# Optimization experiments

Measured on AMD Instinct MI355X. Metric: run time of the kernel, lower is better.

Reference implementation:

```python
import jax, jax.numpy as jnp
import numpy as np

D, H, F, L, V = 768, 4, 1024, 3, 10000
B, TLAB, S = 16, 513, 197
SCALE = 0.02


def setup_inputs() -> dict:
    key = jax.random.key(0)
    ks = jax.random.split(key, 16)
    inp = {
        'labels': jax.random.randint(ks[0], (B, TLAB), 0, V),
        'vision_feats': jax.random.normal(ks[1], (B, S, D), jnp.float32),
        'vis_proj_w': jax.random.normal(ks[2], (D, D), jnp.float32) * SCALE,
        'vis_proj_b': jnp.zeros((D,), jnp.float32),
        'tok_emb': jax.random.normal(ks[3], (V, D), jnp.float32) * SCALE,
        'pos_emb': jax.random.normal(ks[4], (1, 512, D), jnp.float32) * SCALE,
        'sa_w': jax.random.normal(ks[5], (L, 3 * D, D), jnp.float32) * SCALE,
        'sa_b': jnp.zeros((L, 3 * D), jnp.float32),
        'sa_out_w': jax.random.normal(ks[6], (L, D, D), jnp.float32) * SCALE,
        'sa_out_b': jnp.zeros((L, D), jnp.float32),
        'ca_w': jax.random.normal(ks[7], (L, 3 * D, D), jnp.float32) * SCALE,
        'ca_b': jnp.zeros((L, 3 * D), jnp.float32),
        'ca_out_w': jax.random.normal(ks[8], (L, D, D), jnp.float32) * SCALE,
        'ca_out_b': jnp.zeros((L, D), jnp.float32),
        'ln1_g': jnp.ones((L, D), jnp.float32), 'ln1_b': jnp.zeros((L, D), jnp.float32),
        'ln2_g': jnp.ones((L, D), jnp.float32), 'ln2_b': jnp.zeros((L, D), jnp.float32),
        'ln3_g': jnp.ones((L, D), jnp.float32), 'ln3_b': jnp.zeros((L, D), jnp.float32),
        'ff1_w': jax.random.normal(ks[9], (L, F, D), jnp.float32) * SCALE,
        'ff1_b': jnp.zeros((L, F), jnp.float32),
        'ff2_w': jax.random.normal(ks[10], (L, D, F), jnp.float32) * SCALE,
        'ff2_b': jnp.zeros((L, D), jnp.float32),
        'out_w': jax.random.normal(ks[11], (V, D), jnp.float32) * SCALE,
        'out_b': jnp.zeros((V,), jnp.float32),
    }
    return inp


def layer_norm(x, g, b, eps=1e-5):
    m = jnp.mean(x, axis=-1, keepdims=True)
    v = jnp.var(x, axis=-1, keepdims=True)
    return (x - m) / jnp.sqrt(v + eps) * g + b


def mha(qx, kx, vx, w, b, ow, ob, mask):
    # torch nn.MultiheadAttention with packed in_proj [3D, D]
    d = qx.shape[-1]
    hd = d // H
    q = qx @ w[:d].T + b[:d]
    k = kx @ w[d:2 * d].T + b[d:2 * d]
    v = vx @ w[2 * d:].T + b[2 * d:]
    def split(t):
        return t.reshape(t.shape[0], t.shape[1], H, hd).transpose(0, 2, 1, 3)
    q, k, v = split(q), split(k), split(v)  # [B,H,T,hd]
    s = jnp.einsum('bhqd,bhkd->bhqk', q, k) / jnp.sqrt(jnp.asarray(hd, qx.dtype))
    if mask is not None:
        s = s + mask
    a = jax.nn.softmax(s, axis=-1)
    o = jnp.einsum('bhqk,bhkd->bhqd', a, v)
    o = o.transpose(0, 2, 1, 3).reshape(qx.shape[0], qx.shape[1], d)
    return o @ ow.T + ob


def decode(labels, vision_feats, vis_proj_w, vis_proj_b, tok_emb, pos_emb,
           sa_w, sa_b, sa_out_w, sa_out_b, ca_w, ca_b, ca_out_w, ca_out_b,
           ln1_g, ln1_b, ln2_g, ln2_b, ln3_g, ln3_b,
           ff1_w, ff1_b, ff2_w, ff2_b, out_w, out_b):
    mem = vision_feats @ vis_proj_w.T + vis_proj_b          # [B,S,D]
    tgt_tok = labels[:, :-1]                                # [B,T] T=512
    T = tgt_tok.shape[1]
    x = tok_emb[tgt_tok] + pos_emb[:, :T, :]                # [B,T,D]
    # causal additive mask (teacher-forced loop == single full causal pass)
    mask = jnp.where(jnp.tril(jnp.ones((T, T), bool)), 0.0, -jnp.inf).astype(x.dtype)
    for l in range(L):
        x = layer_norm(x + mha(x, x, x, sa_w[l], sa_b[l], sa_out_w[l], sa_out_b[l], mask), ln1_g[l], ln1_b[l])
        x = layer_norm(x + mha(x, mem, mem, ca_w[l], ca_b[l], ca_out_w[l], ca_out_b[l], None), ln2_g[l], ln2_b[l])
        ff = jax.nn.relu(x @ ff1_w[l].T + ff1_b[l]) @ ff2_w[l].T + ff2_b[l]
        x = layer_norm(x + ff, ln3_g[l], ln3_b[l])
    return x @ out_w.T + out_b                              # [B,T,V]


def reference(labels, vision_feats, vis_proj_w, vis_proj_b, tok_emb, pos_emb,
              sa_w, sa_b, sa_out_w, sa_out_b, ca_w, ca_b, ca_out_w, ca_out_b,
              ln1_g, ln1_b, ln2_g, ln2_b, ln3_g, ln3_b,
              ff1_w, ff1_b, ff2_w, ff2_b, out_w, out_b):
    logits = decode(labels, vision_feats, vis_proj_w, vis_proj_b, tok_emb, pos_emb,
                    sa_w, sa_b, sa_out_w, sa_out_b, ca_w, ca_b, ca_out_w, ca_out_b,
                    ln1_g, ln1_b, ln2_g, ln2_b, ln3_g, ln3_b,
                    ff1_w, ff1_b, ff2_w, ff2_b, out_w, out_b)
    return (logits, labels[:, 1:])
```

## Files before the change

kernel.cpp:

```cpp
#include <hip/hip_runtime.h>
#include <hip/hip_fp8.h>

typedef unsigned short u16;
typedef __bf16 bf16x8 __attribute__((ext_vector_type(8)));
typedef float f32x4 __attribute__((ext_vector_type(4)));
typedef unsigned short u16x8 __attribute__((ext_vector_type(8)));
typedef unsigned short u16x4 __attribute__((ext_vector_type(4)));
typedef long i64;

typedef __attribute__((address_space(3))) u16 lds_u16_t;
typedef __attribute__((address_space(1))) const u16 glb_u16_t;
typedef __attribute__((address_space(3))) unsigned char lds_u8_t;
typedef __attribute__((address_space(1))) const unsigned char glb_u8_t;

__device__ __forceinline__ u16 f2bf(float f) {
    union { float f; unsigned u; } v; v.f = f;
    unsigned r = v.u + 0x7FFFu + ((v.u >> 16) & 1u);
    return (u16)(r >> 16);
}
__device__ __forceinline__ float bf2f(u16 h) {
    union { unsigned u; float f; } v; v.u = ((unsigned)h) << 16; return v.f;
}
__device__ __forceinline__ unsigned char f2e4m3(float f) {
    __hip_fp8_e4m3 h(f);
    return (unsigned char)h.__x;
}

struct Cast5 { const float* s[5]; u16* d[5]; long n4[5]; };
__global__ __launch_bounds__(256) void cast5_kernel(Cast5 a) {
    int seg = blockIdx.z;
    const float* s = a.s[seg];
    u16* d = a.d[seg];
    long n4 = a.n4[seg];
    long i = (long)blockIdx.x * 256 + threadIdx.x;
    long stride = (long)gridDim.x * 256;
    for (; i < n4; i += stride) {
        float4 f = reinterpret_cast<const float4*>(s)[i];
        ushort4 o;
        o.x = f2bf(f.x); o.y = f2bf(f.y); o.z = f2bf(f.z); o.w = f2bf(f.w);
        reinterpret_cast<ushort4*>(d)[i] = o;
    }
}
struct CastQ { const float* s[4]; unsigned char* d[4]; long n4[4]; };
__global__ __launch_bounds__(256) void castq_kernel(CastQ a) {
    int seg = blockIdx.z;
    const float* s = a.s[seg];
    unsigned char* d = a.d[seg];
    long n4 = a.n4[seg];
    long i = (long)blockIdx.x * 256 + threadIdx.x;
    long stride = (long)gridDim.x * 256;
    for (; i < n4; i += stride) {
        float4 f = reinterpret_cast<const float4*>(s)[i];
        uchar4 o;
        o.x = f2e4m3(f.x * 256.f); o.y = f2e4m3(f.y * 256.f);
        o.z = f2e4m3(f.z * 256.f); o.w = f2e4m3(f.w * 256.f);
        reinterpret_cast<uchar4*>(d)[i] = o;
    }
}

__global__ __launch_bounds__(256) void embed_kernel(
    const int* __restrict__ labels, const float* __restrict__ tok_emb,
    const float* __restrict__ pos_emb, u16* __restrict__ xb,
    unsigned char* __restrict__ xq, float* __restrict__ lab_out)
{
    int wid = threadIdx.x >> 6, lane = threadIdx.x & 63;
    int r = blockIdx.x * 4 + wid;
    int b = r >> 9, t = r & 511;
    int tok = labels[b * 513 + t];
    if (lane == 0) lab_out[r] = (float)labels[b * 513 + t + 1];
    const float* te = tok_emb + (long)tok * 768;
    const float* pe = pos_emb + (long)t * 768;
    u16* xo = xb + (long)r * 768;
    unsigned char* qo = xq + (long)r * 768;
    int base = lane * 12;
#pragma unroll
    for (int c = 0; c < 3; c++) {
        float4 a = *reinterpret_cast<const float4*>(te + base + c * 4);
        float4 p = *reinterpret_cast<const float4*>(pe + base + c * 4);
        float v0 = a.x + p.x, v1 = a.y + p.y, v2 = a.z + p.z, v3 = a.w + p.w;
        ushort4 o; o.x = f2bf(v0); o.y = f2bf(v1); o.z = f2bf(v2); o.w = f2bf(v3);
        *reinterpret_cast<ushort4*>(xo + base + c * 4) = o;
        uchar4 q; q.x = f2e4m3(v0); q.y = f2e4m3(v1); q.z = f2e4m3(v2); q.w = f2e4m3(v3);
        *reinterpret_cast<uchar4*>(qo + base + c * 4) = q;
    }
}

template<int OB, int RELU, int BM, int MW>
__global__ __launch_bounds__(256, MW) void gemmT(
    const u16* __restrict__ A, int lda, long sAb, long sAh,
    const u16* __restrict__ W, int ldw, long sWb, long sWh,
    const float* __restrict__ bias,
    void* __restrict__ C, int ldc, long sCb, long sCh,
    int M, int N, int K, int NH)
{
    constexpr int MREP = 4;
    constexpr int NREP = (BM == 128) ? 4 : 2;
    __shared__ __align__(16) u16 As0[BM * 32];
    __shared__ __align__(16) u16 As1[BM * 32];
    __shared__ __align__(16) u16 Bs0[128 * 32];
    __shared__ __align__(16) u16 Bs1[128 * 32];

    int z = blockIdx.z, zb = z / NH, zh = z % NH;
    const u16* Ap = A + (long)zb * sAb + (long)zh * sAh;
    const u16* Wp = W + (long)zb * sWb + (long)zh * sWh;
    long coff = (long)zb * sCb + (long)zh * sCh;

    int gx = (int)gridDim.x, gy = (int)gridDim.y;
    int nwg = gx * gy;
    int orig = (int)(blockIdx.y * gridDim.x + blockIdx.x);
    int q = nwg >> 3, r = nwg & 7;
    int xcd = orig & 7, loc = orig >> 3;
    int wg = (xcd < r ? xcd * (q + 1) : r * (q + 1) + (xcd - r) * q) + loc;
    int full = 8 * gy;
    int nsc = (gx + 7) >> 3;
    int sc = wg / full; if (sc > nsc - 1) sc = nsc - 1;
    int rem = wg - sc * full;
    int wdt = gx - sc * 8; if (wdt > 8) wdt = 8;
    int by = rem / wdt, bx = sc * 8 + rem % wdt;

    int m0 = by * BM, n0 = bx * 128;
    int tid = threadIdx.x, wid = tid >> 6, lane = tid & 63;
    int wr = (BM == 128) ? (wid >> 1) * 64 : 0;
    int wc = (BM == 128) ? (wid & 1) * 64 : wid * 32;
    int fr = lane & 15, fk = (lane >> 4) * 8;

    int li0 = wid * 64 + lane;
    int li1 = li0 + 256;
    int r0 = li0 >> 2, c0 = (li0 & 3) * 8;
    int r1 = li1 >> 2, c1 = (li1 & 3) * 8;
    long aoff0 = (long)min(m0 + r0, M - 1) * lda + c0;
    long aoff1 = (BM == 128) ? ((long)min(m0 + r1, M - 1) * lda + c1) : 0;
    long woff0 = (long)min(n0 + r0, N - 1) * ldw + c0;
    long woff1 = (long)min(n0 + r1, N - 1) * ldw + c1;
    char* a0base = (char*)As0 + wid * 1024;
    char* a1base = (char*)As1 + wid * 1024;
    char* b0base = (char*)Bs0 + wid * 1024;
    char* b1base = (char*)Bs1 + wid * 1024;

    f32x4 acc[MREP][NREP] = {};

    auto stage = [&](char* ab, char* bb, int kt) {
        int k0 = kt * 32;
        __builtin_amdgcn_global_load_lds((glb_u16_t*)(Ap + aoff0 + k0), (lds_u16_t*)ab, 16, 0, 0);
        if (BM == 128)
            __builtin_amdgcn_global_load_lds((glb_u16_t*)(Ap + aoff1 + k0), (lds_u16_t*)(ab + 4096), 16, 0, 0);
        __builtin_amdgcn_global_load_lds((glb_u16_t*)(Wp + woff0 + k0), (lds_u16_t*)bb, 16, 0, 0);
        __builtin_amdgcn_global_load_lds((glb_u16_t*)(Wp + woff1 + k0), (lds_u16_t*)(bb + 4096), 16, 0, 0);
    };
    auto compute = [&](const u16* as, const u16* bs) {
        bf16x8 af[MREP], bw[NREP];
#pragma unroll
        for (int m = 0; m < MREP; m++)
            af[m] = *reinterpret_cast<const bf16x8*>(&as[(wr + m * 16 + fr) * 32 + fk]);
#pragma unroll
        for (int n = 0; n < NREP; n++)
            bw[n] = *reinterpret_cast<const bf16x8*>(&bs[(wc + n * 16 + fr) * 32 + fk]);
#pragma unroll
        for (int m = 0; m < MREP; m++)
#pragma unroll
            for (int n = 0; n < NREP; n++)
                acc[m][n] = __builtin_amdgcn_mfma_f32_16x16x32_bf16(af[m], bw[n], acc[m][n], 0, 0, 0);
    };

    int nt = K >> 5;
    stage(a0base, b0base, 0);
    __syncthreads();
    for (int t = 0; t < nt; t += 2) {
        stage(a1base, b1base, t + 1);
        compute(As0, Bs0);
        __syncthreads();
        if (t + 2 < nt) stage(a0base, b0base, t + 2);
        compute(As1, Bs1);
        __syncthreads();
    }

    int crow = (lane >> 4) * 4;
#pragma unroll
    for (int m = 0; m < MREP; m++) {
#pragma unroll
        for (int n = 0; n < NREP; n++) {
            int col = n0 + wc + n * 16 + fr;
            if (col >= N) continue;
            float bv = bias ? bias[col] : 0.f;
            int rbase = m0 + wr + m * 16 + crow;
#pragma unroll
            for (int rr = 0; rr < 4; rr++) {
                int row = rbase + rr;
                if (row >= M) continue;
                float v = acc[m][n][rr] + bv;
                if (RELU) v = fmaxf(v, 0.f);
                long idx = coff + (long)row * ldc + col;
                if (OB) ((u16*)C)[idx] = f2bf(v);
                else    ((float*)C)[idx] = v;
            }
        }
    }
}

template<int OUT, int RELU>
__global__ __launch_bounds__(256, 4) void gemm8(
    const unsigned char* __restrict__ A, int lda,
    const unsigned char* __restrict__ W, int ldw,
    const float* __restrict__ bias, float outscale,
    void* __restrict__ C, int ldc,
    int M, int N, int K)
{
    __shared__ __align__(16) unsigned char As0[128 * 64];
    __shared__ __align__(16) unsigned char As1[128 * 64];
    __shared__ __align__(16) unsigned char Bs0[128 * 64];
    __shared__ __align__(16) unsigned char Bs1[128 * 64];

    int gx = (int)gridDim.x, gy = (int)gridDim.y;
    int nwg = gx * gy;
    int orig = (int)(blockIdx.y * gridDim.x + blockIdx.x);
    int q = nwg >> 3, r = nwg & 7;
    int xcd = orig & 7, loc = orig >> 3;
    int wg = (xcd < r ? xcd * (q + 1) : r * (q + 1) + (xcd - r) * q) + loc;
    int full = 8 * gy;
    int nsc = (gx + 7) >> 3;
    int sc = wg / full; if (sc > nsc - 1) sc = nsc - 1;
    int rem = wg - sc * full;
    int wdt = gx - sc * 8; if (wdt > 8) wdt = 8;
    int by = rem / wdt, bx = sc * 8 + rem % wdt;

    int m0 = by * 128, n0 = bx * 128;
    int tid = threadIdx.x, wid = tid >> 6, lane = tid & 63;
    int wr = (wid >> 1) * 64, wc = (wid & 1) * 64;
    int fr = lane & 15, g8 = (lane >> 4) * 8;

    int li0 = wid * 64 + lane;
    int rs = li0 >> 1;
    int cs = li0 & 1;
    int kc = ((cs ^ (rs >> 2)) & 1) << 4;
    long aoff = (long)min(m0 + rs, M - 1) * lda + kc;
    long woff = (long)min(n0 + rs, N - 1) * ldw + kc;
    char* a0base = (char*)As0 + wid * 1024;
    char* a1base = (char*)As1 + wid * 1024;
    char* b0base = (char*)Bs0 + wid * 1024;
    char* b1base = (char*)Bs1 + wid * 1024;

    f32x4 acc[4][4] = {};

    auto stage = [&](char* ab, char* bb, int kt) {
        int k0 = kt * 64;
        __builtin_amdgcn_global_load_lds((glb_u8_t*)(A + aoff + k0), (lds_u8_t*)ab, 16, 0, 0);
        __builtin_amdgcn_global_load_lds((glb_u8_t*)(A + aoff + k0 + 32), (lds_u8_t*)(ab + 4096), 16, 0, 0);
        __builtin_amdgcn_global_load_lds((glb_u8_t*)(W + woff + k0), (lds_u8_t*)bb, 16, 0, 0);
        __builtin_amdgcn_global_load_lds((glb_u8_t*)(W + woff + k0 + 32), (lds_u8_t*)(bb + 4096), 16, 0, 0);
    };
    int cg = g8 >> 4, go = g8 & 15;
    auto compute = [&](const unsigned char* as, const unsigned char* bs) {
        i64 af[4][2], bw[4][2];
#pragma unroll
        for (int m = 0; m < 4; m++) {
            int rr2 = wr + m * 16 + fr;
            int off = rr2 * 32 + (((cg ^ (rr2 >> 2)) & 1) << 4) + go;
            af[m][0] = *reinterpret_cast<const i64*>(as + off);
            af[m][1] = *reinterpret_cast<const i64*>(as + 4096 + off);
        }
#pragma unroll
        for (int n = 0; n < 4; n++) {
            int rr2 = wc + n * 16 + fr;
            int off = rr2 * 32 + (((cg ^ (rr2 >> 2)) & 1) << 4) + go;
            bw[n][0] = *reinterpret_cast<const i64*>(bs + off);
            bw[n][1] = *reinterpret_cast<const i64*>(bs + 4096 + off);
        }
#pragma unroll
        for (int ks = 0; ks < 2; ks++)
#pragma unroll
            for (int m = 0; m < 4; m++)
#pragma unroll
                for (int n = 0; n < 4; n++)
                    acc[m][n] = __builtin_amdgcn_mfma_f32_16x16x32_fp8_fp8(
                        af[m][ks], bw[n][ks], acc[m][n], 0, 0, 0);
    };

    int nt = K >> 6;
    stage(a0base, b0base, 0);
    __syncthreads();
    for (int t = 0; t < nt; t += 2) {
        stage(a1base, b1base, t + 1);
        compute(As0, Bs0);
        __syncthreads();
        if (t + 2 < nt) stage(a0base, b0base, t + 2);
        compute(As1, Bs1);
        __syncthreads();
    }

    int crow = (lane >> 4) * 4;
#pragma unroll
    for (int m = 0; m < 4; m++) {
#pragma unroll
        for (int n = 0; n < 4; n++) {
            int col = n0 + wc + n * 16 + fr;
            if (col >= N) continue;
            float bv = bias ? bias[col] : 0.f;
            int rbase = m0 + wr + m * 16 + crow;
#pragma unroll
            for (int rr = 0; rr < 4; rr++) {
                int row = rbase + rr;
                if (row >= M) continue;
                float v = acc[m][n][rr] * outscale + bv;
                if (RELU) v = fmaxf(v, 0.f);
                long idx = (long)row * ldc + col;
                if (OUT == 0)      ((float*)C)[idx] = v;
                else if (OUT == 1) ((u16*)C)[idx] = f2bf(v);
                else               ((unsigned char*)C)[idx] = f2e4m3(v);
            }
        }
    }
}

__global__ __launch_bounds__(256) void transpose_pad(
    const u16* __restrict__ V, long sVb, long sVh, int ldv, int NH,
    u16* __restrict__ VT, long sVT, int rowsIn, int Kp)
{
    __shared__ u16 tile[32][33];
    int z = blockIdx.z, zb = z / NH, zh = z % NH;
    const u16* Vp = V + (long)zb * sVb + (long)zh * sVh;
    int k0 = blockIdx.x * 32, d0 = blockIdx.y * 32;
#pragma unroll
    for (int i = 0; i < 4; i++) {
        int k = k0 + threadIdx.y + i * 8;
        int d = d0 + threadIdx.x;
        tile[threadIdx.y + i * 8][threadIdx.x] = (k < rowsIn) ? Vp[(long)k * ldv + d] : (u16)0;
    }
    __syncthreads();
    u16* Op = VT + (long)z * sVT;
#pragma unroll
    for (int i = 0; i < 4; i++) {
        int d = d0 + threadIdx.y + i * 8;
        int k = k0 + threadIdx.x;
        Op[(long)d * Kp + k] = tile[threadIdx.x][threadIdx.y + i * 8];
    }
}

template<int CPL, int CAUSAL>
__global__ __launch_bounds__(256) void softmax2(
    const u16* __restrict__ S, u16* __restrict__ P,
    int ld_in, int valid_in, int ld_out, float scale)
{
    int wid = threadIdx.x >> 6, lane = threadIdx.x & 63;
    long r = (long)blockIdx.x * 4 + wid;
    int q = (int)(r & 511);
    int valid = CAUSAL ? (q + 1) : valid_in;
    const u16* srow = S + r * (long)ld_in;
    u16* prow = P + r * (long)ld_out;
    int base = lane * CPL;
    float v[CPL];
    if constexpr (CPL == 8) {
        u16x8 x = *reinterpret_cast<const u16x8*>(srow + base);
#pragma unroll
        for (int j = 0; j < 8; j++) v[j] = bf2f(x[j]);
    } else {
        u16x4 x = *reinterpret_cast<const u16x4*>(srow + base);
#pragma unroll
        for (int j = 0; j < 4; j++) v[j] = bf2f(x[j]);
    }
    float mx = -3e38f;
#pragma unroll
    for (int j = 0; j < CPL; j++) {
        v[j] *= scale;
        if (base + j < valid) mx = fmaxf(mx, v[j]);
    }
#pragma unroll
    for (int o = 32; o; o >>= 1) mx = fmaxf(mx, __shfl_xor(mx, o, 64));
    float e[CPL], s = 0.f;
#pragma unroll
    for (int j = 0; j < CPL; j++) {
        e[j] = (base + j < valid) ? __expf(v[j] - mx) : 0.f;
        s += e[j];
    }
#pragma unroll
    for (int o = 32; o; o >>= 1) s += __shfl_xor(s, o, 64);
    float inv = 1.f / s;
    if constexpr (CPL == 8) {
        u16x8 o8;
#pragma unroll
        for (int j = 0; j < 8; j++) o8[j] = f2bf(e[j] * inv);
        *reinterpret_cast<u16x8*>(prow + base) = o8;
    } else {
        u16x4 o4;
#pragma unroll
        for (int j = 0; j < 4; j++) o4[j] = f2bf(e[j] * inv);
        *reinterpret_cast<u16x4*>(prow + base) = o4;
    }
}

__global__ __launch_bounds__(256) void ln_kernel(
    const u16* __restrict__ xin, const u16* __restrict__ subb,
    const float* __restrict__ g, const float* __restrict__ bta,
    u16* __restrict__ xout, unsigned char* __restrict__ q8)
{
    int wid = threadIdx.x >> 6, lane = threadIdx.x & 63;
    long r = (long)blockIdx.x * 4 + wid;
    const u16* a = xin + r * 768;
    const u16* s = subb + r * 768;
    int base = lane * 12;
    float v[12];
    float sum = 0.f;
#pragma unroll
    for (int c = 0; c < 3; c++) {
        ushort4 av = *reinterpret_cast<const ushort4*>(a + base + c * 4);
        ushort4 sv = *reinterpret_cast<const ushort4*>(s + base + c * 4);
        v[c*4+0] = bf2f(av.x) + bf2f(sv.x);
        v[c*4+1] = bf2f(av.y) + bf2f(sv.y);
        v[c*4+2] = bf2f(av.z) + bf2f(sv.z);
        v[c*4+3] = bf2f(av.w) + bf2f(sv.w);
        sum += v[c*4+0] + v[c*4+1] + v[c*4+2] + v[c*4+3];
    }
#pragma unroll
    for (int o = 32; o; o >>= 1) sum += __shfl_xor(sum, o, 64);
    float mean = sum * (1.f / 768.f);
    float vs = 0.f;
#pragma unroll
    for (int j = 0; j < 12; j++) { float t = v[j] - mean; vs += t * t; }
#pragma unroll
    for (int o = 32; o; o >>= 1) vs += __shfl_xor(vs, o, 64);
    float rstd = rsqrtf(vs * (1.f / 768.f) + 1e-5f);
    u16* xo = xout + r * 768;
    unsigned char* qo = q8 ? q8 + r * 768 : nullptr;
#pragma unroll
    for (int c = 0; c < 3; c++) {
        float4 gv = *reinterpret_cast<const float4*>(g + base + c * 4);
        float4 bv = *reinterpret_cast<const float4*>(bta + base + c * 4);
        float y0 = (v[c*4+0] - mean) * rstd * gv.x + bv.x;
        float y1 = (v[c*4+1] - mean) * rstd * gv.y + bv.y;
        float y2 = (v[c*4+2] - mean) * rstd * gv.z + bv.z;
        float y3 = (v[c*4+3] - mean) * rstd * gv.w + bv.w;
        ushort4 o; o.x = f2bf(y0); o.y = f2bf(y1); o.z = f2bf(y2); o.w = f2bf(y3);
        *reinterpret_cast<ushort4*>(xo + base + c * 4) = o;
        if (qo) {
            uchar4 qb; qb.x = f2e4m3(y0); qb.y = f2e4m3(y1); qb.z = f2e4m3(y2); qb.w = f2e4m3(y3);
            *reinterpret_cast<uchar4*>(qo + base + c * 4) = qb;
        }
    }
}

static void g128_bf(hipStream_t st, const u16* A, int lda, const u16* W, int ldw,
                    const float* bias, void* C, int ldc, int M, int N, int K) {
    dim3 g((N + 127) / 128, (M + 127) / 128, 1), b(256, 1, 1);
    gemmT<1,0,128,4><<<g,b,0,st>>>(A,lda,0,0,W,ldw,0,0,bias,C,ldc,0,0,M,N,K,1);
}
static void g64_bf(hipStream_t st, bool relu, const u16* A, int lda, const u16* W, int ldw,
                   const float* bias, void* C, int ldc, int M, int N, int K) {
    dim3 g((N + 127) / 128, (M + 63) / 64, 1), b(256, 1, 1);
    if (relu) gemmT<1,1,64,4><<<g,b,0,st>>>(A,lda,0,0,W,ldw,0,0,bias,C,ldc,0,0,M,N,K,1);
    else      gemmT<1,0,64,4><<<g,b,0,st>>>(A,lda,0,0,W,ldw,0,0,bias,C,ldc,0,0,M,N,K,1);
}
static void gbat(hipStream_t st,
    const u16* A, int lda, long sAb, long sAh,
    const u16* W, int ldw, long sWb, long sWh,
    void* C, int ldc, long sCb, long sCh,
    int M, int N, int K, int Z, int NH) {
    dim3 g((N + 127) / 128, (M + 127) / 128, Z), b(256, 1, 1);
    gemmT<1,0,128,4><<<g,b,0,st>>>(A,lda,sAb,sAh,W,ldw,sWb,sWh,nullptr,C,ldc,sCb,sCh,M,N,K,NH);
}
template<int OUT, int RELU>
static void g8(hipStream_t st, const unsigned char* A, int lda, const unsigned char* W, int ldw,
               const float* bias, void* C, int ldc, int M, int N, int K) {
    dim3 g((N + 127) / 128, (M + 127) / 128, 1), b(256, 1, 1);
    gemm8<OUT,RELU><<<g,b,0,st>>>(A,lda,W,ldw,bias,1.f/256.f,C,ldc,M,N,K);
}

extern "C" void kernel_launch(void* const* d_in, const int* in_sizes, int n_in,
                              void* d_out, int out_size, void* d_ws, size_t ws_size,
                              hipStream_t stream)
{
    const int*   labels = (const int*)  d_in[0];
    const float* vision = (const float*)d_in[1];
    const float* vpw    = (const float*)d_in[2];
    const float* vpb    = (const float*)d_in[3];
    const float* temb   = (const float*)d_in[4];
    const float* pemb   = (const float*)d_in[5];
    const float* saw    = (const float*)d_in[6];
    const float* sab    = (const float*)d_in[7];
    const float* saow   = (const float*)d_in[8];
    const float* saob   = (const float*)d_in[9];
    const float* caw    = (const float*)d_in[10];
    const float* cab    = (const float*)d_in[11];
    const float* caow   = (const float*)d_in[12];
    const float* caob   = (const float*)d_in[13];
    const float* ln1g   = (const float*)d_in[14];
    const float* ln1b   = (const float*)d_in[15];
    const float* ln2g   = (const float*)d_in[16];
    const float* ln2b   = (const float*)d_in[17];
    const float* ln3g   = (const float*)d_in[18];
    const float* ln3b   = (const float*)d_in[19];
    const float* f1w    = (const float*)d_in[20];
    const float* f1b    = (const float*)d_in[21];
    const float* f2w    = (const float*)d_in[22];
    const float* f2b    = (const float*)d_in[23];
    const float* ow     = (const float*)d_in[24];
    const float* ob     = (const float*)d_in[25];
    (void)in_sizes; (void)n_in; (void)out_size;

    char* p = (char*)d_ws;
    auto alloc = [&](long elems, int esz) -> char* {
        char* r = p; p += ((long)elems * esz + 255) & ~255L; return r;
    };
    u16* wb_vp  = (u16*)alloc(768L*768, 2);
    u16* wb_sao = (u16*)alloc(3L*768*768, 2);
    u16* wb_ca  = (u16*)alloc(3L*2304*768, 2);
    u16* wb_cao = (u16*)alloc(3L*768*768, 2);
    unsigned char* w8_sa = (unsigned char*)alloc(3L*2304*768, 1);
    unsigned char* w8_f1 = (unsigned char*)alloc(3L*1024*768, 1);
    unsigned char* w8_f2 = (unsigned char*)alloc(3L*768*1024, 1);
    unsigned char* w8_ow = (unsigned char*)alloc(10000L*768, 1);
    unsigned char* xq    = (unsigned char*)alloc(8192L*768, 1);
    unsigned char* h8    = (unsigned char*)alloc(8192L*1024, 1);
    u16* vis_b  = (u16*)alloc(3152L*768, 2);
    u16* mem_b  = (u16*)alloc(3152L*768, 2);
    u16* xb     = (u16*)alloc(8192L*768, 2);
    u16* qkv    = (u16*)alloc(8192L*2304, 2);
    u16* q_bf   = qkv;
    u16* kv_bf  = qkv + 8192L*768;
    u16* scb    = (u16*)alloc(64L*512*512, 2);
    u16* pr     = (u16*)alloc(64L*512*512, 2);
    u16* vt     = (u16*)alloc(64L*192*512, 2);
    u16* attn   = (u16*)alloc(8192L*768, 2);
    u16* subb   = (u16*)alloc(8192L*768, 2);
    if ((size_t)(p - (char*)d_ws) > ws_size) return;

    Cast5 c5;
    c5.s[0] = vpw;    c5.d[0] = wb_vp;  c5.n4[0] = 768L*768/4;
    c5.s[1] = saow;   c5.d[1] = wb_sao; c5.n4[1] = 3L*768*768/4;
    c5.s[2] = caw;    c5.d[2] = wb_ca;  c5.n4[2] = 3L*2304*768/4;
    c5.s[3] = caow;   c5.d[3] = wb_cao; c5.n4[3] = 3L*768*768/4;
    c5.s[4] = vision; c5.d[4] = vis_b;  c5.n4[4] = 3152L*768/4;
    cast5_kernel<<<dim3(512, 1, 5), dim3(256), 0, stream>>>(c5);
    CastQ cq;
    cq.s[0] = saw; cq.d[0] = w8_sa; cq.n4[0] = 3L*2304*768/4;
    cq.s[1] = f1w; cq.d[1] = w8_f1; cq.n4[1] = 3L*1024*768/4;
    cq.s[2] = f2w; cq.d[2] = w8_f2; cq.n4[2] = 3L*768*1024/4;
    cq.s[3] = ow;  cq.d[3] = w8_ow; cq.n4[3] = 10000L*768/4;
    castq_kernel<<<dim3(512, 1, 4), dim3(256), 0, stream>>>(cq);

    embed_kernel<<<dim3(2048), dim3(256), 0, stream>>>(labels, temb, pemb, xb, xq,
                                                       (float*)d_out + 81920000L);

    g64_bf(stream, false, vis_b, 768, wb_vp, 768, vpb, mem_b, 768, 3152, 768, 768);

    const float scale = 0.07216878364870323f;

    for (int l = 0; l < 3; l++) {
        g8<1,0>(stream, xq, 768, w8_sa + (long)l*2304*768, 768, sab + l*2304,
                qkv, 2304, 8192, 2304, 768);
        transpose_pad<<<dim3(16,6,64), dim3(32,8), 0, stream>>>(
            qkv + 1536, 512L*2304, 192L, 2304, 4, vt, 192L*512, 512, 512);
        gbat(stream, qkv, 2304, 512L*2304, 192, qkv + 768, 2304, 512L*2304, 192,
             scb, 512, 4L*512*512, 512L*512, 512, 512, 192, 64, 4);
        softmax2<8,1><<<dim3(8192), dim3(256), 0, stream>>>(scb, pr, 512, 512, 512, scale);
        gbat(stream, pr, 512, 4L*512*512, 512L*512, vt, 512, 4L*192*512, 192L*512,
             attn, 768, 512L*768, 192, 512, 192, 512, 64, 4);
        g64_bf(stream, false, attn, 768, wb_sao + (long)l*768*768, 768,
               saob + l*768, subb, 768, 8192, 768, 768);
        ln_kernel<<<dim3(2048), dim3(256), 0, stream>>>(xb, subb, ln1g + l*768, ln1b + l*768,
                                                        xb, nullptr);

        const u16* Wca = wb_ca + (long)l*2304*768;
        g64_bf(stream, false, xb, 768, Wca, 768, cab + l*2304, q_bf, 768, 8192, 768, 768);
        g64_bf(stream, false, mem_b, 768, Wca + 768L*768, 768, cab + l*2304 + 768,
               kv_bf, 1536, 3152, 1536, 768);
        transpose_pad<<<dim3(8,6,64), dim3(32,8), 0, stream>>>(
            kv_bf + 768, 197L*1536, 192L, 1536, 4, vt, 192L*256, 197, 256);
        gbat(stream, q_bf, 768, 512L*768, 192, kv_bf, 1536, 197L*1536, 192,
             scb, 224, 4L*512*224, 512L*224, 512, 197, 192, 64, 4);
        softmax2<4,0><<<dim3(8192), dim3(256), 0, stream>>>(scb, pr, 224, 197, 256, scale);
        gbat(stream, pr, 256, 4L*512*256, 512L*256, vt, 256, 4L*192*256, 192L*256,
             attn, 768, 512L*768, 192, 512, 192, 256, 64, 4);
        g64_bf(stream, false, attn, 768, wb_cao + (long)l*768*768, 768,
               caob + l*768, subb, 768, 8192, 768, 768);
        ln_kernel<<<dim3(2048), dim3(256), 0, stream>>>(xb, subb, ln2g + l*768, ln2b + l*768,
                                                        xb, xq);

        g8<2,1>(stream, xq, 768, w8_f1 + (long)l*1024*768, 768, f1b + l*1024,
                h8, 1024, 8192, 1024, 768);
        g8<1,0>(stream, h8, 1024, w8_f2 + (long)l*768*1024, 1024, f2b + l*768,
                subb, 768, 8192, 768, 1024);
        ln_kernel<<<dim3(2048), dim3(256), 0, stream>>>(xb, subb, ln3g + l*768, ln3b + l*768,
                                                        xb, xq);
    }

    g8<0,0>(stream, xq, 768, w8_ow, 768, ob, (float*)d_out, 10000, 8192, 10000, 768);
}
```

Baseline: 1.276 ms.

## Move remaining bf16 projection GEMMs to FP8 and fuse V-transpose into QKV epilogue

Converts the vision projection, self-attention output, cross-attention Q/KV and output projections from bf16 to FP8 GEMMs. All weights and the vision features are quantized in a single cast kernel. The attention PV GEMM now writes FP8 output directly so the following out-projection can consume it. The QKV GEMM epilogue also writes the transposed V, removing a separate transpose kernel, and a BM=64 variant is added to the FP8 GEMM for the narrower matrices. This cuts memory traffic and kernel launches at the cost of more quantization error in several layers.

```diff
diff --git a/kernel.cpp b/kernel.cpp
--- a/kernel.cpp
+++ b/kernel.cpp
@@ -26,34 +26,20 @@
     return (unsigned char)h.__x;
 }
 
-struct Cast5 { const float* s[5]; u16* d[5]; long n4[5]; };
-__global__ __launch_bounds__(256) void cast5_kernel(Cast5 a) {
-    int seg = blockIdx.z;
-    const float* s = a.s[seg];
-    u16* d = a.d[seg];
-    long n4 = a.n4[seg];
-    long i = (long)blockIdx.x * 256 + threadIdx.x;
-    long stride = (long)gridDim.x * 256;
-    for (; i < n4; i += stride) {
-        float4 f = reinterpret_cast<const float4*>(s)[i];
-        ushort4 o;
-        o.x = f2bf(f.x); o.y = f2bf(f.y); o.z = f2bf(f.z); o.w = f2bf(f.w);
-        reinterpret_cast<ushort4*>(d)[i] = o;
-    }
-}
-struct CastQ { const float* s[4]; unsigned char* d[4]; long n4[4]; };
+struct CastQ { const float* s[9]; unsigned char* d[9]; long n4[9]; float mul[9]; };
 __global__ __launch_bounds__(256) void castq_kernel(CastQ a) {
     int seg = blockIdx.z;
     const float* s = a.s[seg];
     unsigned char* d = a.d[seg];
     long n4 = a.n4[seg];
+    float mul = a.mul[seg];
     long i = (long)blockIdx.x * 256 + threadIdx.x;
     long stride = (long)gridDim.x * 256;
     for (; i < n4; i += stride) {
         float4 f = reinterpret_cast<const float4*>(s)[i];
         uchar4 o;
-        o.x = f2e4m3(f.x * 256.f); o.y = f2e4m3(f.y * 256.f);
-        o.z = f2e4m3(f.z * 256.f); o.w = f2e4m3(f.w * 256.f);
+        o.x = f2e4m3(f.x * mul); o.y = f2e4m3(f.y * mul);
+        o.z = f2e4m3(f.z * mul); o.w = f2e4m3(f.w * mul);
         reinterpret_cast<uchar4*>(d)[i] = o;
     }
 }
@@ -85,18 +71,15 @@
     }
 }
 
-template<int OB, int RELU, int BM, int MW>
-__global__ __launch_bounds__(256, MW) void gemmT(
+template<int OUT>
+__global__ __launch_bounds__(256, 4) void gemmT(
     const u16* __restrict__ A, int lda, long sAb, long sAh,
     const u16* __restrict__ W, int ldw, long sWb, long sWh,
-    const float* __restrict__ bias,
     void* __restrict__ C, int ldc, long sCb, long sCh,
     int M, int N, int K, int NH)
 {
-    constexpr int MREP = 4;
-    constexpr int NREP = (BM == 128) ? 4 : 2;
-    __shared__ __align__(16) u16 As0[BM * 32];
-    __shared__ __align__(16) u16 As1[BM * 32];
+    __shared__ __align__(16) u16 As0[128 * 32];
+    __shared__ __align__(16) u16 As1[128 * 32];
     __shared__ __align__(16) u16 Bs0[128 * 32];
     __shared__ __align__(16) u16 Bs1[128 * 32];
 
@@ -118,10 +101,9 @@
     int wdt = gx - sc * 8; if (wdt > 8) wdt = 8;
     int by = rem / wdt, bx = sc * 8 + rem % wdt;
 
-    int m0 = by * BM, n0 = bx * 128;
+    int m0 = by * 128, n0 = bx * 128;
     int tid = threadIdx.x, wid = tid >> 6, lane = tid & 63;
-    int wr = (BM == 128) ? (wid >> 1) * 64 : 0;
-    int wc = (BM == 128) ? (wid & 1) * 64 : wid * 32;
+    int wr = (wid >> 1) * 64, wc = (wid & 1) * 64;
     int fr = lane & 15, fk = (lane >> 4) * 8;
 
     int li0 = wid * 64 + lane;
@@ -129,7 +111,7 @@
     int r0 = li0 >> 2, c0 = (li0 & 3) * 8;
     int r1 = li1 >> 2, c1 = (li1 & 3) * 8;
     long aoff0 = (long)min(m0 + r0, M - 1) * lda + c0;
-    long aoff1 = (BM == 128) ? ((long)min(m0 + r1, M - 1) * lda + c1) : 0;
+    long aoff1 = (long)min(m0 + r1, M - 1) * lda + c1;
     long woff0 = (long)min(n0 + r0, N - 1) * ldw + c0;
     long woff1 = (long)min(n0 + r1, N - 1) * ldw + c1;
     char* a0base = (char*)As0 + wid * 1024;
@@ -137,28 +119,27 @@
     char* b0base = (char*)Bs0 + wid * 1024;
     char* b1base = (char*)Bs1 + wid * 1024;
 
-    f32x4 acc[MREP][NREP] = {};
+    f32x4 acc[4][4] = {};
 
     auto stage = [&](char* ab, char* bb, int kt) {
         int k0 = kt * 32;
         __builtin_amdgcn_global_load_lds((glb_u16_t*)(Ap + aoff0 + k0), (lds_u16_t*)ab, 16, 0, 0);
-        if (BM == 128)
-            __builtin_amdgcn_global_load_lds((glb_u16_t*)(Ap + aoff1 + k0), (lds_u16_t*)(ab + 4096), 16, 0, 0);
+        __builtin_amdgcn_global_load_lds((glb_u16_t*)(Ap + aoff1 + k0), (lds_u16_t*)(ab + 4096), 16, 0, 0);
         __builtin_amdgcn_global_load_lds((glb_u16_t*)(Wp + woff0 + k0), (lds_u16_t*)bb, 16, 0, 0);
         __builtin_amdgcn_global_load_lds((glb_u16_t*)(Wp + woff1 + k0), (lds_u16_t*)(bb + 4096), 16, 0, 0);
     };
     auto compute = [&](const u16* as, const u16* bs) {
-        bf16x8 af[MREP], bw[NREP];
-#pragma unroll
-        for (int m = 0; m < MREP; m++)
+        bf16x8 af[4], bw[4];
+#pragma unroll
+        for (int m = 0; m < 4; m++)
             af[m] = *reinterpret_cast<const bf16x8*>(&as[(wr + m * 16 + fr) * 32 + fk]);
 #pragma unroll
-        for (int n = 0; n < NREP; n++)
+        for (int n = 0; n < 4; n++)
             bw[n] = *reinterpret_cast<const bf16x8*>(&bs[(wc + n * 16 + fr) * 32 + fk]);
 #pragma unroll
-        for (int m = 0; m < MREP; m++)
-#pragma unroll
-            for (int n = 0; n < NREP; n++)
+        for (int m = 0; m < 4; m++)
+#pragma unroll
+            for (int n = 0; n < 4; n++)
                 acc[m][n] = __builtin_amdgcn_mfma_f32_16x16x32_bf16(af[m], bw[n], acc[m][n], 0, 0, 0);
     };
 
@@ -176,37 +157,37 @@
 
     int crow = (lane >> 4) * 4;
 #pragma unroll
-    for (int m = 0; m < MREP; m++) {
-#pragma unroll
-        for (int n = 0; n < NREP; n++) {
+    for (int m = 0; m < 4; m++) {
+#pragma unroll
+        for (int n = 0; n < 4; n++) {
             int col = n0 + wc + n * 16 + fr;
             if (col >= N) continue;
-            float bv = bias ? bias[col] : 0.f;
             int rbase = m0 + wr + m * 16 + crow;
 #pragma unroll
             for (int rr = 0; rr < 4; rr++) {
                 int row = rbase + rr;
                 if (row >= M) continue;
-                float v = acc[m][n][rr] + bv;
-                if (RELU) v = fmaxf(v, 0.f);
+                float v = acc[m][n][rr];
                 long idx = coff + (long)row * ldc + col;
-                if (OB) ((u16*)C)[idx] = f2bf(v);
-                else    ((float*)C)[idx] = v;
+                if (OUT == 1) ((u16*)C)[idx] = f2bf(v);
+                else          ((unsigned char*)C)[idx] = f2e4m3(v);
             }
         }
     }
 }
 
-template<int OUT, int RELU>
+template<int OUT, int RELU, int BM, int FUSEVT>
 __global__ __launch_bounds__(256, 4) void gemm8(
     const unsigned char* __restrict__ A, int lda,
     const unsigned char* __restrict__ W, int ldw,
     const float* __restrict__ bias, float outscale,
-    void* __restrict__ C, int ldc,
+    void* __restrict__ C, int ldc, u16* __restrict__ vt,
     int M, int N, int K)
 {
-    __shared__ __align__(16) unsigned char As0[128 * 64];
-    __shared__ __align__(16) unsigned char As1[128 * 64];
+    constexpr int NREP = (BM == 128) ? 4 : 2;
+    constexpr int AHALF = (BM == 128) ? 4096 : 2048;
+    __shared__ __align__(16) unsigned char As0[BM * 64];
+    __shared__ __align__(16) unsigned char As1[BM * 64];
     __shared__ __align__(16) unsigned char Bs0[128 * 64];
     __shared__ __align__(16) unsigned char Bs1[128 * 64];
 
@@ -223,43 +204,55 @@
     int wdt = gx - sc * 8; if (wdt > 8) wdt = 8;
     int by = rem / wdt, bx = sc * 8 + rem % wdt;
 
-    int m0 = by * 128, n0 = bx * 128;
+    int m0 = by * BM, n0 = bx * 128;
     int tid = threadIdx.x, wid = tid >> 6, lane = tid & 63;
-    int wr = (wid >> 1) * 64, wc = (wid & 1) * 64;
-    int fr = lane & 15, g8 = (lane >> 4) * 8;
+    int wr = (BM == 128) ? (wid >> 1) * 64 : 0;
+    int wc = (BM == 128) ? (wid & 1) * 64 : wid * 32;
+    int fr = lane & 15, gk = (lane >> 4) * 8;
 
     int li0 = wid * 64 + lane;
-    int rs = li0 >> 1;
-    int cs = li0 & 1;
-    int kc = ((cs ^ (rs >> 2)) & 1) << 4;
-    long aoff = (long)min(m0 + rs, M - 1) * lda + kc;
-    long woff = (long)min(n0 + rs, N - 1) * ldw + kc;
+    int rsW = li0 >> 1, csW = li0 & 1;
+    int kcW = ((csW ^ (rsW >> 2)) & 1) << 4;
+    long woff = (long)min(n0 + rsW, N - 1) * ldw + kcW;
+    long aoff;
+    if constexpr (BM == 128) {
+        aoff = (long)min(m0 + rsW, M - 1) * lda + kcW;
+    } else {
+        int halfA = li0 >> 7;
+        int rsA = (li0 >> 1) & 63, csA = li0 & 1;
+        int kcA = ((csA ^ (rsA >> 2)) & 1) << 4;
+        aoff = (long)min(m0 + rsA, M - 1) * lda + halfA * 32 + kcA;
+    }
     char* a0base = (char*)As0 + wid * 1024;
     char* a1base = (char*)As1 + wid * 1024;
     char* b0base = (char*)Bs0 + wid * 1024;
     char* b1base = (char*)Bs1 + wid * 1024;
 
-    f32x4 acc[4][4] = {};
+    f32x4 acc[4][NREP] = {};
 
     auto stage = [&](char* ab, char* bb, int kt) {
         int k0 = kt * 64;
-        __builtin_amdgcn_global_load_lds((glb_u8_t*)(A + aoff + k0), (lds_u8_t*)ab, 16, 0, 0);
-        __builtin_amdgcn_global_load_lds((glb_u8_t*)(A + aoff + k0 + 32), (lds_u8_t*)(ab + 4096), 16, 0, 0);
+        if constexpr (BM == 128) {
+            __builtin_amdgcn_global_load_lds((glb_u8_t*)(A + aoff + k0), (lds_u8_t*)ab, 16, 0, 0);
+            __builtin_amdgcn_global_load_lds((glb_u8_t*)(A + aoff + k0 + 32), (lds_u8_t*)(ab + 4096), 16, 0, 0);
+        } else {
+            __builtin_amdgcn_global_load_lds((glb_u8_t*)(A + aoff + k0), (lds_u8_t*)ab, 16, 0, 0);
+        }
         __builtin_amdgcn_global_load_lds((glb_u8_t*)(W + woff + k0), (lds_u8_t*)bb, 16, 0, 0);
         __builtin_amdgcn_global_load_lds((glb_u8_t*)(W + woff + k0 + 32), (lds_u8_t*)(bb + 4096), 16, 0, 0);
     };
-    int cg = g8 >> 4, go = g8 & 15;
+    int cg = gk >> 4, go = gk & 15;
     auto compute = [&](const unsigned char* as, const unsigned char* bs) {
-        i64 af[4][2], bw[4][2];
+        i64 af[4][2], bw[NREP][2];
 #pragma unroll
         for (int m = 0; m < 4; m++) {
             int rr2 = wr + m * 16 + fr;
             int off = rr2 * 32 + (((cg ^ (rr2 >> 2)) & 1) << 4) + go;
             af[m][0] = *reinterpret_cast<const i64*>(as + off);
-            af[m][1] = *reinterpret_cast<const i64*>(as + 4096 + off);
+            af[m][1] = *reinterpret_cast<const i64*>(as + AHALF + off);
         }
 #pragma unroll
-        for (int n = 0; n < 4; n++) {
+        for (int n = 0; n < NREP; n++) {
             int rr2 = wc + n * 16 + fr;
             int off = rr2 * 32 + (((cg ^ (rr2 >> 2)) & 1) << 4) + go;
             bw[n][0] = *reinterpret_cast<const i64*>(bs + off);
@@ -270,7 +263,7 @@
 #pragma unroll
             for (int m = 0; m < 4; m++)
 #pragma unroll
-                for (int n = 0; n < 4; n++)
+                for (int n = 0; n < NREP; n++)
                     acc[m][n] = __builtin_amdgcn_mfma_f32_16x16x32_fp8_fp8(
                         af[m][ks], bw[n][ks], acc[m][n], 0, 0, 0);
     };
@@ -291,21 +284,33 @@
 #pragma unroll
     for (int m = 0; m < 4; m++) {
 #pragma unroll
-        for (int n = 0; n < 4; n++) {
+        for (int n = 0; n < NREP; n++) {
             int col = n0 + wc + n * 16 + fr;
             if (col >= N) continue;
             float bv = bias ? bias[col] : 0.f;
             int rbase = m0 + wr + m * 16 + crow;
+            float vv[4];
 #pragma unroll
             for (int rr = 0; rr < 4; rr++) {
                 int row = rbase + rr;
                 if (row >= M) continue;
                 float v = acc[m][n][rr] * outscale + bv;
                 if (RELU) v = fmaxf(v, 0.f);
+                vv[rr] = v;
                 long idx = (long)row * ldc + col;
                 if (OUT == 0)      ((float*)C)[idx] = v;
                 else if (OUT == 1) ((u16*)C)[idx] = f2bf(v);
                 else               ((unsigned char*)C)[idx] = f2e4m3(v);
+            }
+            if constexpr (FUSEVT) {
+                if (col >= 1536) {
+                    int tt = col - 1536;
+                    int h = tt / 192, d = tt - h * 192;
+                    int b = rbase >> 9, k0 = rbase & 511;
+                    ushort4 o;
+                    o.x = f2bf(vv[0]); o.y = f2bf(vv[1]); o.z = f2bf(vv[2]); o.w = f2bf(vv[3]);
+                    *reinterpret_cast<ushort4*>(vt + ((long)((b << 2) + h) * 192 + d) * 512 + k0) = o;
+                }
             }
         }
     }
@@ -419,7 +424,7 @@
     for (int o = 32; o; o >>= 1) vs += __shfl_xor(vs, o, 64);
     float rstd = rsqrtf(vs * (1.f / 768.f) + 1e-5f);
     u16* xo = xout + r * 768;
-    unsigned char* qo = q8 ? q8 + r * 768 : nullptr;
+    unsigned char* qo = q8 + r * 768;
 #pragma unroll
     for (int c = 0; c < 3; c++) {
         float4 gv = *reinterpret_cast<const float4*>(g + base + c * 4);
@@ -430,37 +435,30 @@
         float y3 = (v[c*4+3] - mean) * rstd * gv.w + bv.w;
         ushort4 o; o.x = f2bf(y0); o.y = f2bf(y1); o.z = f2bf(y2); o.w = f2bf(y3);
         *reinterpret_cast<ushort4*>(xo + base + c * 4) = o;
-        if (qo) {
-            uchar4 qb; qb.x = f2e4m3(y0); qb.y = f2e4m3(y1); qb.z = f2e4m3(y2); qb.w = f2e4m3(y3);
-            *reinterpret_cast<uchar4*>(qo + base + c * 4) = qb;
-        }
-    }
-}
-
-static void g128_bf(hipStream_t st, const u16* A, int lda, const u16* W, int ldw,
-                    const float* bias, void* C, int ldc, int M, int N, int K) {
-    dim3 g((N + 127) / 128, (M + 127) / 128, 1), b(256, 1, 1);
-    gemmT<1,0,128,4><<<g,b,0,st>>>(A,lda,0,0,W,ldw,0,0,bias,C,ldc,0,0,M,N,K,1);
-}
-static void g64_bf(hipStream_t st, bool relu, const u16* A, int lda, const u16* W, int ldw,
-                   const float* bias, void* C, int ldc, int M, int N, int K) {
-    dim3 g((N + 127) / 128, (M + 63) / 64, 1), b(256, 1, 1);
-    if (relu) gemmT<1,1,64,4><<<g,b,0,st>>>(A,lda,0,0,W,ldw,0,0,bias,C,ldc,0,0,M,N,K,1);
-    else      gemmT<1,0,64,4><<<g,b,0,st>>>(A,lda,0,0,W,ldw,0,0,bias,C,ldc,0,0,M,N,K,1);
-}
+        uchar4 qb; qb.x = f2e4m3(y0); qb.y = f2e4m3(y1); qb.z = f2e4m3(y2); qb.w = f2e4m3(y3);
+        *reinterpret_cast<uchar4*>(qo + base + c * 4) = qb;
+    }
+}
+
+template<int OUT>
 static void gbat(hipStream_t st,
     const u16* A, int lda, long sAb, long sAh,
     const u16* W, int ldw, long sWb, long sWh,
     void* C, int ldc, long sCb, long sCh,
     int M, int N, int K, int Z, int NH) {
     dim3 g((N + 127) / 128, (M + 127) / 128, Z), b(256, 1, 1);
-    gemmT<1,0,128,4><<<g,b,0,st>>>(A,lda,sAb,sAh,W,ldw,sWb,sWh,nullptr,C,ldc,sCb,sCh,M,N,K,NH);
-}
-template<int OUT, int RELU>
+    gemmT<OUT><<<g,b,0,st>>>(A,lda,sAb,sAh,W,ldw,sWb,sWh,C,ldc,sCb,sCh,M,N,K,NH);
+}
+template<int OUT, int RELU, int BM>
 static void g8(hipStream_t st, const unsigned char* A, int lda, const unsigned char* W, int ldw,
                const float* bias, void* C, int ldc, int M, int N, int K) {
-    dim3 g((N + 127) / 128, (M + 127) / 128, 1), b(256, 1, 1);
-    gemm8<OUT,RELU><<<g,b,0,st>>>(A,lda,W,ldw,bias,1.f/256.f,C,ldc,M,N,K);
+    dim3 g((N + 127) / 128, (M + BM - 1) / BM, 1), b(256, 1, 1);
+    gemm8<OUT,RELU,BM,0><<<g,b,0,st>>>(A,lda,W,ldw,bias,1.f/256.f,C,ldc,nullptr,M,N,K);
+}
+static void g8qkv(hipStream_t st, const unsigned char* A, const unsigned char* W,
+                  const float* bias, u16* C, u16* vt) {
+    dim3 g(18, 64, 1), b(256, 1, 1);
+    gemm8<1,0,128,1><<<g,b,0,st>>>(A,768,W,768,bias,1.f/256.f,C,2304,vt,8192,2304,768);
 }
 
 extern "C" void kernel_launch(void* const* d_in, const int* in_sizes, int n_in,
@@ -499,88 +497,83 @@
     auto alloc = [&](long elems, int esz) -> char* {
         char* r = p; p += ((long)elems * esz + 255) & ~255L; return r;
     };
-    u16* wb_vp  = (u16*)alloc(768L*768, 2);
-    u16* wb_sao = (u16*)alloc(3L*768*768, 2);
-    u16* wb_ca  = (u16*)alloc(3L*2304*768, 2);
-    u16* wb_cao = (u16*)alloc(3L*768*768, 2);
-    unsigned char* w8_sa = (unsigned char*)alloc(3L*2304*768, 1);
-    unsigned char* w8_f1 = (unsigned char*)alloc(3L*1024*768, 1);
-    unsigned char* w8_f2 = (unsigned char*)alloc(3L*768*1024, 1);
-    unsigned char* w8_ow = (unsigned char*)alloc(10000L*768, 1);
-    unsigned char* xq    = (unsigned char*)alloc(8192L*768, 1);
-    unsigned char* h8    = (unsigned char*)alloc(8192L*1024, 1);
-    u16* vis_b  = (u16*)alloc(3152L*768, 2);
-    u16* mem_b  = (u16*)alloc(3152L*768, 2);
-    u16* xb     = (u16*)alloc(8192L*768, 2);
-    u16* qkv    = (u16*)alloc(8192L*2304, 2);
-    u16* q_bf   = qkv;
-    u16* kv_bf  = qkv + 8192L*768;
-    u16* scb    = (u16*)alloc(64L*512*512, 2);
-    u16* pr     = (u16*)alloc(64L*512*512, 2);
-    u16* vt     = (u16*)alloc(64L*192*512, 2);
-    u16* attn   = (u16*)alloc(8192L*768, 2);
-    u16* subb   = (u16*)alloc(8192L*768, 2);
+    unsigned char* w8_sa  = (unsigned char*)alloc(3L*2304*768, 1);
+    unsigned char* w8_ca  = (unsigned char*)alloc(3L*2304*768, 1);
+    unsigned char* w8_sao = (unsigned char*)alloc(3L*768*768, 1);
+    unsigned char* w8_cao = (unsigned char*)alloc(3L*768*768, 1);
+    unsigned char* w8_f1  = (unsigned char*)alloc(3L*1024*768, 1);
+    unsigned char* w8_f2  = (unsigned char*)alloc(3L*768*1024, 1);
+    unsigned char* w8_ow  = (unsigned char*)alloc(10000L*768, 1);
+    unsigned char* w8_vp  = (unsigned char*)alloc(768L*768, 1);
+    unsigned char* vis8   = (unsigned char*)alloc(3152L*768, 1);
+    unsigned char* mem8   = (unsigned char*)alloc(3152L*768, 1);
+    unsigned char* xq     = (unsigned char*)alloc(8192L*768, 1);
+    unsigned char* h8     = (unsigned char*)alloc(8192L*1024, 1);
+    unsigned char* attn8  = (unsigned char*)alloc(8192L*768, 1);
+    u16* xb   = (u16*)alloc(8192L*768, 2);
+    u16* qkv  = (u16*)alloc(8192L*2304, 2);
+    u16* q_bf = qkv;
+    u16* kv_bf = qkv + 8192L*768;
+    u16* scb  = (u16*)alloc(64L*512*512, 2);
+    u16* pr   = (u16*)alloc(64L*512*512, 2);
+    u16* vt   = (u16*)alloc(64L*192*512, 2);
+    u16* subb = (u16*)alloc(8192L*768, 2);
     if ((size_t)(p - (char*)d_ws) > ws_size) return;
 
-    Cast5 c5;
-    c5.s[0] = vpw;    c5.d[0] = wb_vp;  c5.n4[0] = 768L*768/4;
-    c5.s[1] = saow;   c5.d[1] = wb_sao; c5.n4[1] = 3L*768*768/4;
-    c5.s[2] = caw;    c5.d[2] = wb_ca;  c5.n4[2] = 3L*2304*768/4;
-    c5.s[3] = caow;   c5.d[3] = wb_cao; c5.n4[3] = 3L*768*768/4;
-    c5.s[4] = vision; c5.d[4] = vis_b;  c5.n4[4] = 3152L*768/4;
-    cast5_kernel<<<dim3(512, 1, 5), dim3(256), 0, stream>>>(c5);
     CastQ cq;
-    cq.s[0] = saw; cq.d[0] = w8_sa; cq.n4[0] = 3L*2304*768/4;
-    cq.s[1] = f1w; cq.d[1] = w8_f1; cq.n4[1] = 3L*1024*768/4;
-    cq.s[2] = f2w; cq.d[2] = w8_f2; cq.n4[2] = 3L*768*1024/4;
-    cq.s[3] = ow;  cq.d[3] = w8_ow; cq.n4[3] = 10000L*768/4;
-    castq_kernel<<<dim3(512, 1, 4), dim3(256), 0, stream>>>(cq);
+    cq.s[0] = saw;    cq.d[0] = w8_sa;  cq.n4[0] = 3L*2304*768/4;  cq.mul[0] = 256.f;
+    cq.s[1] = caw;    cq.d[1] = w8_ca;  cq.n4[1] = 3L*2304*768/4;  cq.mul[1] = 256.f;
+    cq.s[2] = saow;   cq.d[2] = w8_sao; cq.n4[2] = 3L*768*768/4;   cq.mul[2] = 256.f;
+    cq.s[3] = caow;   cq.d[3] = w8_cao; cq.n4[3] = 3L*768*768/4;   cq.mul[3] = 256.f;
+    cq.s[4] = f1w;    cq.d[4] = w8_f1;  cq.n4[4] = 3L*1024*768/4;  cq.mul[4] = 256.f;
+    cq.s[5] = f2w;    cq.d[5] = w8_f2;  cq.n4[5] = 3L*768*1024/4;  cq.mul[5] = 256.f;
+    cq.s[6] = ow;     cq.d[6] = w8_ow;  cq.n4[6] = 10000L*768/4;   cq.mul[6] = 256.f;
+    cq.s[7] = vpw;    cq.d[7] = w8_vp;  cq.n4[7] = 768L*768/4;     cq.mul[7] = 256.f;
+    cq.s[8] = vision; cq.d[8] = vis8;   cq.n4[8] = 3152L*768/4;    cq.mul[8] = 1.f;
+    castq_kernel<<<dim3(512, 1, 9), dim3(256), 0, stream>>>(cq);
 
     embed_kernel<<<dim3(2048), dim3(256), 0, stream>>>(labels, temb, pemb, xb, xq,
                                                        (float*)d_out + 81920000L);
 
-    g64_bf(stream, false, vis_b, 768, wb_vp, 768, vpb, mem_b, 768, 3152, 768, 768);
+    g8<2,0,64>(stream, vis8, 768, w8_vp, 768, vpb, mem8, 768, 3152, 768, 768);
 
     const float scale = 0.07216878364870323f;
 
     for (int l = 0; l < 3; l++) {
-        g8<1,0>(stream, xq, 768, w8_sa + (long)l*2304*768, 768, sab + l*2304,
-                qkv, 2304, 8192, 2304, 768);
-        transpose_pad<<<dim3(16,6,64), dim3(32,8), 0, stream>>>(
-            qkv + 1536, 512L*2304, 192L, 2304, 4, vt, 192L*512, 512, 512);
-        gbat(stream, qkv, 2304, 512L*2304, 192, qkv + 768, 2304, 512L*2304, 192,
-             scb, 512, 4L*512*512, 512L*512, 512, 512, 192, 64, 4);
+        g8qkv(stream, xq, w8_sa + (long)l*2304*768, sab + l*2304, qkv, vt);
+        gbat<1>(stream, qkv, 2304, 512L*2304, 192, qkv + 768, 2304, 512L*2304, 192,
+                scb, 512, 4L*512*512, 512L*512, 512, 512, 192, 64, 4);
         softmax2<8,1><<<dim3(8192), dim3(256), 0, stream>>>(scb, pr, 512, 512, 512, scale);
-        gbat(stream, pr, 512, 4L*512*512, 512L*512, vt, 512, 4L*192*512, 192L*512,
-             attn, 768, 512L*768, 192, 512, 192, 512, 64, 4);
-        g64_bf(stream, false, attn, 768, wb_sao + (long)l*768*768, 768,
-               saob + l*768, subb, 768, 8192, 768, 768);
+        gbat<2>(stream, pr, 512, 4L*512*512, 512L*512, vt, 512, 4L*192*512, 192L*512,
+                attn8, 768, 512L*768, 192, 512, 192, 512, 64, 4);
+        g8<1,0,64>(stream, attn8, 768, w8_sao + (long)l*768*768, 768,
+                   saob + l*768, subb, 768, 8192, 768, 768);
         ln_kernel<<<dim3(2048), dim3(256), 0, stream>>>(xb, subb, ln1g + l*768, ln1b + l*768,
-                                                        xb, nullptr);
-
-        const u16* Wca = wb_ca + (long)l*2304*768;
-        g64_bf(stream, false, xb, 768, Wca, 768, cab + l*2304, q_bf, 768, 8192, 768, 768);
-        g64_bf(stream, false, mem_b, 768, Wca + 768L*768, 768, cab + l*2304 + 768,
-               kv_bf, 1536, 3152, 1536, 768);
+                                                        xb, xq);
+
+        g8<1,0,64>(stream, xq, 768, w8_ca + (long)l*2304*768, 768,
+                   cab + l*2304, q_bf, 768, 8192, 768, 768);
+        g8<1,0,64>(stream, mem8, 768, w8_ca + (long)l*2304*768 + 768L*768, 768,
+                   cab + l*2304 + 768, kv_bf, 1536, 3152, 1536, 768);
         transpose_pad<<<dim3(8,6,64), dim3(32,8), 0, stream>>>(
             kv_bf + 768, 197L*1536, 192L, 1536, 4, vt, 192L*256, 197, 256);
-        gbat(stream, q_bf, 768, 512L*768, 192, kv_bf, 1536, 197L*1536, 192,
-             scb, 224, 4L*512*224, 512L*224, 512, 197, 192, 64, 4);
+        gbat<1>(stream, q_bf, 768, 512L*768, 192, kv_bf, 1536, 197L*1536, 192,
+                scb, 224, 4L*512*224, 512L*224, 512, 197, 192, 64, 4);
         softmax2<4,0><<<dim3(8192), dim3(256), 0, stream>>>(scb, pr, 224, 197, 256, scale);
-        gbat(stream, pr, 256, 4L*512*256, 512L*256, vt, 256, 4L*192*256, 192L*256,
-             attn, 768, 512L*768, 192, 512, 192, 256, 64, 4);
-        g64_bf(stream, false, attn, 768, wb_cao + (long)l*768*768, 768,
-               caob + l*768, subb, 768, 8192, 768, 768);
+        gbat<2>(stream, pr, 256, 4L*512*256, 512L*256, vt, 256, 4L*192*256, 192L*256,
+                attn8, 768, 512L*768, 192, 512, 192, 256, 64, 4);
+        g8<1,0,64>(stream, attn8, 768, w8_cao + (long)l*768*768, 768,
+                   caob + l*768, subb, 768, 8192, 768, 768);
         ln_kernel<<<dim3(2048), dim3(256), 0, stream>>>(xb, subb, ln2g + l*768, ln2b + l*768,
                                                         xb, xq);
 
-        g8<2,1>(stream, xq, 768, w8_f1 + (long)l*1024*768, 768, f1b + l*1024,
-                h8, 1024, 8192, 1024, 768);
-        g8<1,0>(stream, h8, 1024, w8_f2 + (long)l*768*1024, 1024, f2b + l*768,
-                subb, 768, 8192, 768, 1024);
+        g8<2,1,128>(stream, xq, 768, w8_f1 + (long)l*1024*768, 768, f1b + l*1024,
+                    h8, 1024, 8192, 1024, 768);
+        g8<1,0,64>(stream, h8, 1024, w8_f2 + (long)l*768*1024, 1024, f2b + l*768,
+                   subb, 768, 8192, 768, 1024);
         ln_kernel<<<dim3(2048), dim3(256), 0, stream>>>(xb, subb, ln3g + l*768, ln3b + l*768,
                                                         xb, xq);
     }
 
-    g8<0,0>(stream, xq, 768, w8_ow, 768, ob, (float*)d_out, 10000, 8192, 10000, 768);
-}
+    g8<0,0,128>(stream, xq, 768, w8_ow, 768, ob, (float*)d_out, 10000, 8192, 10000, 768);
+}
```

Result: faster. 1.109 ms (-13.1%).
